# Kernel optimization log

Hardware: AMD Instinct MI355X
Metric: run time of the kernel (lower is better)

## Reference

```python
import jax, jax.numpy as jnp
import numpy as np

E = 8388608          # total edges across batch
G = 2048             # num_graphs
LARGE_NEG = -1.0e9
SCORE_EPS = 1e-6     # self.score_eps
STOP_BIAS = 0.0      # self.stop_logit_bias
RAND_PROB = 0.1      # self.random_action_prob (training)
TEMP = 1.0           # policy_temperature (>= MIN_TEMPERATURE)
PROB_EPS = 1e-12
EPS = float(np.finfo(np.float32).eps)  # torch.finfo(edge_tokens.dtype).eps


def setup_inputs() -> dict:
    key = jax.random.key(0)
    k1, k2, k3, k4, k5 = jax.random.split(key, 5)
    edge_scores = jax.random.uniform(k1, (E,), dtype=jnp.float32)
    edge_residual = jax.random.normal(k2, (E,), dtype=jnp.float32)
    stop_residual = jax.random.normal(k3, (G,), dtype=jnp.float32)
    valid_edges = jax.random.bernoulli(k4, 0.9, (E,))
    edge_batch = jnp.sort(jax.random.randint(k5, (E,), 0, G, dtype=jnp.int32))
    return {"edge_scores": edge_scores, "edge_residual": edge_residual,
            "stop_residual": stop_residual, "valid_edges": valid_edges,
            "edge_batch": edge_batch}


def _segment_log_probs(edge_logits, stop_logits, valid, edge_batch, temp):
    """Faithful port of _log_probs_from_logits: per-graph stable softmax over
    a ragged set of edge logits plus one stop logit per graph."""
    masked = jnp.where(valid, edge_logits, LARGE_NEG)
    scaled = masked / temp                                   # [E]
    sstop = stop_logits / temp                               # [G]
    max_edge = jax.ops.segment_max(scaled, edge_batch, num_segments=G)
    has_edge = jax.ops.segment_sum(jnp.ones_like(scaled), edge_batch, num_segments=G) > 0
    max_edge = jnp.where(has_edge, max_edge, LARGE_NEG)
    max_joint = jnp.maximum(max_edge, sstop)                 # [G]
    exp_edges = jax.ops.segment_sum(jnp.exp(scaled - max_joint[edge_batch]),
                                    edge_batch, num_segments=G)
    exp_stop = jnp.exp(sstop - max_joint)
    log_denom = max_joint + jnp.log(exp_edges + exp_stop + EPS)  # [G]
    log_edge = jnp.where(valid, scaled - log_denom[edge_batch], LARGE_NEG)
    log_stop = sstop - log_denom
    return log_edge, log_stop


def reference(edge_scores, edge_residual, stop_residual, valid_edges, edge_batch):
    # base (prior) distribution from GNN edge scores + stop bias
    base_edge_logits = jnp.log(jnp.maximum(edge_scores, SCORE_EPS))
    base_stop_logits = jnp.full((G,), STOP_BIAS, dtype=jnp.float32)
    base_log_edge, base_log_stop = _segment_log_probs(
        base_edge_logits, base_stop_logits, valid_edges, edge_batch, 1.0)
    # combine with policy residuals and renormalize at temperature
    combined_edge = base_log_edge + edge_residual
    combined_stop = base_log_stop + stop_residual
    clean_log_edge, clean_log_stop = _segment_log_probs(
        combined_edge, combined_stop, valid_edges, edge_batch, TEMP)
    clean_edge_prob = jnp.exp(clean_log_edge)
    clean_stop_prob = jnp.exp(clean_log_stop)
    # uniform random-action mixing
    valid_counts = jax.ops.segment_sum(valid_edges.astype(jnp.float32),
                                       edge_batch, num_segments=G)
    total_actions = jnp.maximum(valid_counts + 1.0, 1.0)     # [G]
    uniform_edge = jnp.where(valid_edges, 1.0 / total_actions[edge_batch], 0.0)
    uniform_stop = 1.0 / total_actions
    sample_edge = (1.0 - RAND_PROB) * clean_edge_prob + RAND_PROB * uniform_edge
    sample_stop = (1.0 - RAND_PROB) * clean_stop_prob + RAND_PROB * uniform_stop
    log_sample_edge = jnp.where(valid_edges,
                                jnp.log(jnp.maximum(sample_edge, PROB_EPS)),
                                LARGE_NEG)
    log_sample_stop = jnp.log(jnp.maximum(sample_stop, PROB_EPS))
    # greedy action per graph: best edge vs stop
    best_val = jax.ops.segment_max(log_sample_edge, edge_batch, num_segments=G)
    idx = jnp.arange(E, dtype=jnp.int32)
    cand = jnp.where(log_sample_edge == best_val[edge_batch], idx, E)
    best_idx = jax.ops.segment_min(cand, edge_batch, num_segments=G)   # [G]
    counts = jax.ops.segment_sum(jnp.ones((E,), jnp.int32), edge_batch, num_segments=G)
    stop_indices = jnp.cumsum(counts)                         # edge_ptr[1:]
    take_stop = log_sample_stop >= best_val
    actions = jnp.where(take_stop, stop_indices, best_idx)
    chosen_edge_lp = clean_log_edge[jnp.minimum(best_idx, E - 1)]
    log_pf = jnp.where(take_stop, clean_log_stop, chosen_edge_lp)     # [G]
    return clean_log_edge, clean_log_stop, actions, log_pf
```

## Files before the change

### kernel.cpp

```cpp
#include <hip/hip_runtime.h>
#include <math.h>
#include <climits>

#define BLOCK 256
#define NCHUNK 5
#define REGCAP (NCHUNK * BLOCK * 4)
#define LARGE_NEG (-1.0e9f)
#define SCORE_EPS 1e-6f
#define RANDP 0.1f
#define PROB_EPS 1e-12f
#define F32EPS 1.1920928955078125e-7f

typedef float f4v __attribute__((ext_vector_type(4)));

__global__ void gfn_setup(const int* __restrict__ batch, int E, int G,
                          int* __restrict__ ptr,
                          const unsigned int* __restrict__ vwords, int nwords,
                          int nbytes, int* __restrict__ flag, int nbPtr) {
  if ((int)blockIdx.x < nbPtr) {
    int g = blockIdx.x * BLOCK + threadIdx.x;
    if (g > G) return;
    int lo = 0, hi = E;
    while (lo < hi) {
      int mid = (lo + hi) >> 1;
      if (batch[mid] < g) lo = mid + 1; else hi = mid;
    }
    ptr[g] = lo;
  } else {
    int c = 0;
    for (int i = threadIdx.x; i < nwords; i += BLOCK) {
      unsigned int w = vwords[i];
      c += ((w & 0x000000FFu) != 0) + ((w & 0x0000FF00u) != 0) +
           ((w & 0x00FF0000u) != 0) + ((w & 0xFF000000u) != 0);
    }
#pragma unroll
    for (int o = 32; o >= 1; o >>= 1) c += __shfl_xor(c, o);
    __shared__ int part[4];
    if ((threadIdx.x & 63) == 0) part[threadIdx.x >> 6] = c;
    __syncthreads();
    if (threadIdx.x == 0) {
      int t = part[0] + part[1] + part[2] + part[3];
      flag[0] = (2 * t > nbytes) ? 1 : 0;
    }
  }
}

__global__ __launch_bounds__(BLOCK) void
gfn_main(const float* __restrict__ scores,
         const float* __restrict__ resid,
         const float* __restrict__ stop_resid,
         const void* __restrict__ validp,
         const int* __restrict__ ptr,
         const int* __restrict__ flag,
         float* __restrict__ out, int E, int G) {
  __shared__ float redf[16];
  __shared__ int redi[4];

  const int g = blockIdx.x;
  const int start = ptr[g];
  const int end = ptr[g + 1];
  const bool byteFmt = (flag[0] != 0);
  const unsigned char* vb = (const unsigned char*)validp;
  const int* vi = (const int*)validp;
  const int abase = start & ~3;

  if ((E & 3) == 0 && (end - abase) <= REGCAP) {
    float c[NCHUNK][4];
    const int t4 = (int)threadIdx.x * 4;

    float smax = 0.f, ssum = 0.f, vc = 0.f, tmax = LARGE_NEG;
#pragma unroll
    for (int j = 0; j < NCHUNK; ++j) {
      const int e0 = abase + j * (BLOCK * 4) + t4;
      if (e0 < end) {
        const float4 s4 = *(const float4*)(scores + e0);
        const float4 r4 = *(const float4*)(resid + e0);
        int vv[4];
        if (byteFmt) {
          const uchar4 u = *(const uchar4*)(vb + e0);
          vv[0] = u.x; vv[1] = u.y; vv[2] = u.z; vv[3] = u.w;
        } else {
          const int4 u = *(const int4*)(vi + e0);
          vv[0] = u.x; vv[1] = u.y; vv[2] = u.z; vv[3] = u.w;
        }
        const float ss[4] = {s4.x, s4.y, s4.z, s4.w};
        const float rr[4] = {r4.x, r4.y, r4.z, r4.w};
#pragma unroll
        for (int k = 0; k < 4; ++k) {
          const int e = e0 + k;
          const bool ok = (e >= start) & (e < end) & (vv[k] != 0);
          const float w = ok ? fmaxf(ss[k], SCORE_EPS) : 0.f;
          smax = fmaxf(smax, w);
          ssum += w;
          vc += ok ? 1.f : 0.f;
          const float t = ok ? (__logf(w) + rr[k]) : LARGE_NEG;
          c[j][k] = t;
          tmax = fmaxf(tmax, t);
        }
      } else {
#pragma unroll
        for (int k = 0; k < 4; ++k) c[j][k] = LARGE_NEG;
      }
    }
#pragma unroll
    for (int o = 32; o >= 1; o >>= 1) {
      smax = fmaxf(smax, __shfl_xor(smax, o));
      ssum += __shfl_xor(ssum, o);
      vc += __shfl_xor(vc, o);
      tmax = fmaxf(tmax, __shfl_xor(tmax, o));
    }
    if ((threadIdx.x & 63) == 0) {
      const int w = threadIdx.x >> 6;
      redf[w] = smax; redf[4 + w] = ssum; redf[8 + w] = vc; redf[12 + w] = tmax;
    }
    __syncthreads();
    smax = fmaxf(fmaxf(redf[0], redf[1]), fmaxf(redf[2], redf[3]));
    ssum = (redf[4] + redf[5]) + (redf[6] + redf[7]);
    vc = (redf[8] + redf[9]) + (redf[10] + redf[11]);
    tmax = fmaxf(fmaxf(redf[12], redf[13]), fmaxf(redf[14], redf[15]));
    __syncthreads();

    const float M = fmaxf(smax, 1.f);
    const float invM = 1.f / M;
    const float ld1 = __logf(M) + __logf(ssum * invM + invM + F32EPS);
    const float m2 = tmax - ld1;
    const float ss2 = stop_resid[g] - ld1;
    const float mj2 = fmaxf(m2, ss2);
    const float off2 = ld1 + mj2;

    float s2 = 0.f;
#pragma unroll
    for (int j = 0; j < NCHUNK; ++j)
#pragma unroll
      for (int k = 0; k < 4; ++k) s2 += __expf(c[j][k] - off2);
#pragma unroll
    for (int o = 32; o >= 1; o >>= 1) s2 += __shfl_xor(s2, o);
    if ((threadIdx.x & 63) == 0) redf[threadIdx.x >> 6] = s2;
    __syncthreads();
    s2 = (redf[0] + redf[1]) + (redf[2] + redf[3]);
    __syncthreads();
    const float ld2 = mj2 + __logf(s2 + __expf(ss2 - mj2) + F32EPS);
    const float clean_stop = ss2 - ld2;
    const float invt = 1.f / fmaxf(vc + 1.f, 1.f);
    const float off3 = ld1 + ld2;

    float bv = -INFINITY;
    int bi = INT_MAX;
#pragma unroll
    for (int j = 0; j < NCHUNK; ++j) {
      const int e0 = abase + j * (BLOCK * 4) + t4;
      if (e0 < end) {
        float ov[4];
#pragma unroll
        for (int k = 0; k < 4; ++k) {
          const int e = e0 + k;
          const float t = c[j][k];
          const bool v = (t != LARGE_NEG);
          ov[k] = v ? (t - off3) : LARGE_NEG;
          if (v && (t > bv || (t == bv && e < bi))) { bv = t; bi = e; }
        }
        if (e0 >= start && e0 + 4 <= end) {
          f4v val; val.x = ov[0]; val.y = ov[1]; val.z = ov[2]; val.w = ov[3];
          __builtin_nontemporal_store(val, (f4v*)(out + e0));
        } else {
#pragma unroll
          for (int k = 0; k < 4; ++k) {
            const int e = e0 + k;
            if (e >= start && e < end)
              __builtin_nontemporal_store(ov[k], out + e);
          }
        }
      }
    }
#pragma unroll
    for (int o = 32; o >= 1; o >>= 1) {
      const float v2 = __shfl_xor(bv, o);
      const int i2 = __shfl_xor(bi, o);
      if (v2 > bv || (v2 == bv && i2 < bi)) { bv = v2; bi = i2; }
    }
    if ((threadIdx.x & 63) == 0) {
      const int w = threadIdx.x >> 6;
      redf[w] = bv; redi[w] = bi;
    }
    __syncthreads();
    if (threadIdx.x == 0) {
      bv = redf[0]; bi = redi[0];
      for (int w = 1; w < 4; ++w) {
        if (redf[w] > bv || (redf[w] == bv && redi[w] < bi)) {
          bv = redf[w]; bi = redi[w];
        }
      }
      const bool anyvalid = (bi != INT_MAX);
      const float wclean = bv - off3;
      float bvls = LARGE_NEG;
      if (anyvalid) {
        const float p = (1.f - RANDP) * __expf(wclean) + RANDP * invt;
        bvls = __logf(fmaxf(p, PROB_EPS));
      }
      const float ssp = (1.f - RANDP) * __expf(clean_stop) + RANDP * invt;
      const float lss = __logf(fmaxf(ssp, PROB_EPS));
      const bool take_stop = (lss >= bvls);
      out[E + g]         = clean_stop;
      out[E + G + g]     = take_stop ? (float)end : (float)bi;
      out[E + 2 * G + g] = take_stop ? clean_stop : wclean;
    }
    return;
  }

  const int n = end - start;
  auto load_l = [&](int e) -> float {
    float s = scores[e];
    int v = byteFmt ? (int)vb[e] : vi[e];
    return v ? __logf(fmaxf(s, SCORE_EPS)) : LARGE_NEG;
  };

  float m1 = LARGE_NEG, vc = 0.f;
  for (int i = threadIdx.x; i < n; i += BLOCK) {
    float l = load_l(start + i);
    m1 = fmaxf(m1, l);
    if (l != LARGE_NEG) vc += 1.f;
  }
#pragma unroll
  for (int o = 32; o >= 1; o >>= 1) {
    m1 = fmaxf(m1, __shfl_xor(m1, o));
    vc += __shfl_xor(vc, o);
  }
  if ((threadIdx.x & 63) == 0) {
    const int w = threadIdx.x >> 6;
    redf[w] = m1; redf[4 + w] = vc;
  }
  __syncthreads();
  m1 = fmaxf(fmaxf(redf[0], redf[1]), fmaxf(redf[2], redf[3]));
  vc = (redf[4] + redf[5]) + (redf[6] + redf[7]);
  __syncthreads();

  const float mj1 = fmaxf(m1, 0.f);
  float s1 = 0.f;
  for (int i = threadIdx.x; i < n; i += BLOCK)
    s1 += __expf(load_l(start + i) - mj1);
#pragma unroll
  for (int o = 32; o >= 1; o >>= 1) s1 += __shfl_xor(s1, o);
  if ((threadIdx.x & 63) == 0) redf[threadIdx.x >> 6] = s1;
  __syncthreads();
  s1 = (redf[0] + redf[1]) + (redf[2] + redf[3]);
  __syncthreads();
  const float ld1 = mj1 + __logf(s1 + __expf(-mj1) + F32EPS);

  float m2 = LARGE_NEG;
  for (int i = threadIdx.x; i < n; i += BLOCK) {
    float l = load_l(start + i);
    float cc = (l != LARGE_NEG) ? (l - ld1 + resid[start + i]) : LARGE_NEG;
    m2 = fmaxf(m2, cc);
  }
#pragma unroll
  for (int o = 32; o >= 1; o >>= 1) m2 = fmaxf(m2, __shfl_xor(m2, o));
  if ((threadIdx.x & 63) == 0) redf[threadIdx.x >> 6] = m2;
  __syncthreads();
  m2 = fmaxf(fmaxf(redf[0], redf[1]), fmaxf(redf[2], redf[3]));
  __syncthreads();

  const float ss2 = stop_resid[g] - ld1;
  const float mj2 = fmaxf(m2, ss2);
  float s2 = 0.f;
  for (int i = threadIdx.x; i < n; i += BLOCK) {
    float l = load_l(start + i);
    float cc = (l != LARGE_NEG) ? (l - ld1 + resid[start + i]) : LARGE_NEG;
    s2 += __expf(cc - mj2);
  }
#pragma unroll
  for (int o = 32; o >= 1; o >>= 1) s2 += __shfl_xor(s2, o);
  if ((threadIdx.x & 63) == 0) redf[threadIdx.x >> 6] = s2;
  __syncthreads();
  s2 = (redf[0] + redf[1]) + (redf[2] + redf[3]);
  __syncthreads();
  const float ld2 = mj2 + __logf(s2 + __expf(ss2 - mj2) + F32EPS);
  const float clean_stop = ss2 - ld2;
  const float invt = 1.f / fmaxf(vc + 1.f, 1.f);

  float bv = -INFINITY; int bi = INT_MAX; float bc = 0.f;
  for (int i = threadIdx.x; i < n; i += BLOCK) {
    const int e = start + i;
    float l = load_l(e);
    float cc = (l != LARGE_NEG) ? (l - ld1 + resid[e]) : LARGE_NEG;
    const bool v = (cc != LARGE_NEG);
    const float clean = cc - ld2;
    out[e] = v ? clean : LARGE_NEG;
    float ls;
    if (v) {
      const float p = (1.f - RANDP) * __expf(clean) + RANDP * invt;
      ls = __logf(fmaxf(p, PROB_EPS));
    } else ls = LARGE_NEG;
    if (ls > bv || (ls == bv && e < bi)) { bv = ls; bi = e; bc = clean; }
  }
#pragma unroll
  for (int o = 32; o >= 1; o >>= 1) {
    const float v2 = __shfl_xor(bv, o);
    const int i2 = __shfl_xor(bi, o);
    const float c2 = __shfl_xor(bc, o);
    if (v2 > bv || (v2 == bv && i2 < bi)) { bv = v2; bi = i2; bc = c2; }
  }
  if ((threadIdx.x & 63) == 0) {
    const int w = threadIdx.x >> 6;
    redf[w] = bv; redf[4 + w] = bc; redi[w] = bi;
  }
  __syncthreads();
  if (threadIdx.x == 0) {
    bv = redf[0]; bi = redi[0]; bc = redf[4];
    for (int w = 1; w < 4; ++w) {
      if (redf[w] > bv || (redf[w] == bv && redi[w] < bi)) {
        bv = redf[w]; bi = redi[w]; bc = redf[4 + w];
      }
    }
    const float ssp = (1.f - RANDP) * __expf(clean_stop) + RANDP * invt;
    const float lss = __logf(fmaxf(ssp, PROB_EPS));
    const bool take_stop = (lss >= bv);
    out[E + g]         = clean_stop;
    out[E + G + g]     = take_stop ? (float)end : (float)bi;
    out[E + 2 * G + g] = take_stop ? clean_stop : bc;
  }
}

extern "C" void kernel_launch(void* const* d_in, const int* in_sizes, int n_in,
                              void* d_out, int out_size, void* d_ws, size_t ws_size,
                              hipStream_t stream) {
  const float* scores     = (const float*)d_in[0];
  const float* resid      = (const float*)d_in[1];
  const float* stop_resid = (const float*)d_in[2];
  const void*  validp     = d_in[3];
  const int*   batch      = (const int*)d_in[4];
  const int E = in_sizes[0];
  const int G = in_sizes[2];

  int* flag = (int*)d_ws;
  int* ptr  = (int*)d_ws + 64;
  float* out = (float*)d_out;

  int sample_bytes = (E < 8192) ? (E & ~3) : 8192;
  int nbPtr = (G + 1 + BLOCK - 1) / BLOCK;
  gfn_setup<<<nbPtr + 1, BLOCK, 0, stream>>>(batch, E, G, ptr,
                                             (const unsigned int*)validp,
                                             sample_bytes / 4, sample_bytes,
                                             flag, nbPtr);
  gfn_main<<<G, BLOCK, 0, stream>>>(scores, resid, stop_resid, validp, ptr,
                                    flag, out, E, G);
}
```

Baseline: 37.15 us.

## Fuse segment-boundary search and format detection into main kernel

Removes the separate setup kernel. Each block now finds its own segment boundaries with a 64-way wave-cooperative search over the sorted batch array, and detects the validity format from a smaller sample inside the block. Loads are hoisted ahead of compute with a compact validity bitmask, launch bounds request higher occupancy, and nontemporal stores become plain stores. This saves one kernel launch and a dependency, but every block repeats the boundary search and format sampling, and the changed occupancy hint may raise register pressure.

```diff
diff --git a/kernel.cpp b/kernel.cpp
--- a/kernel.cpp
+++ b/kernel.cpp
@@ -11,95 +11,116 @@
 #define PROB_EPS 1e-12f
 #define F32EPS 1.1920928955078125e-7f
 
-typedef float f4v __attribute__((ext_vector_type(4)));
-
-__global__ void gfn_setup(const int* __restrict__ batch, int E, int G,
-                          int* __restrict__ ptr,
-                          const unsigned int* __restrict__ vwords, int nwords,
-                          int nbytes, int* __restrict__ flag, int nbPtr) {
-  if ((int)blockIdx.x < nbPtr) {
-    int g = blockIdx.x * BLOCK + threadIdx.x;
-    if (g > G) return;
-    int lo = 0, hi = E;
-    while (lo < hi) {
-      int mid = (lo + hi) >> 1;
-      if (batch[mid] < g) lo = mid + 1; else hi = mid;
-    }
-    ptr[g] = lo;
-  } else {
-    int c = 0;
-    for (int i = threadIdx.x; i < nwords; i += BLOCK) {
-      unsigned int w = vwords[i];
-      c += ((w & 0x000000FFu) != 0) + ((w & 0x0000FF00u) != 0) +
-           ((w & 0x00FF0000u) != 0) + ((w & 0xFF000000u) != 0);
-    }
-#pragma unroll
-    for (int o = 32; o >= 1; o >>= 1) c += __shfl_xor(c, o);
-    __shared__ int part[4];
-    if ((threadIdx.x & 63) == 0) part[threadIdx.x >> 6] = c;
-    __syncthreads();
-    if (threadIdx.x == 0) {
-      int t = part[0] + part[1] + part[2] + part[3];
-      flag[0] = (2 * t > nbytes) ? 1 : 0;
-    }
-  }
+__device__ __forceinline__ int wave_lower_bound(const int* __restrict__ batch,
+                                                int E, int target) {
+  const int lane = (int)(threadIdx.x & 63);
+  long long lo = 0, hi = E;
+  for (int it = 0; it < 12 && hi > lo; ++it) {
+    const long long W = hi - lo;
+    const long long step = (W + 63) >> 6;
+    const long long p = lo + (long long)lane * step;
+    bool pred = false;
+    if (p < hi) pred = (batch[p] < target);
+    const unsigned long long m = __ballot(pred);
+    const int c = __popcll(m);
+    if (c == 0) { hi = lo; break; }
+    const long long plast = lo + (long long)(c - 1) * step;
+    const long long pnext = lo + (long long)c * step;
+    lo = plast + 1;
+    hi = (c < 64 && pnext < hi) ? pnext : hi;
+  }
+  return (int)lo;
 }
 
-__global__ __launch_bounds__(BLOCK) void
+__global__ __launch_bounds__(BLOCK, 4) void
 gfn_main(const float* __restrict__ scores,
          const float* __restrict__ resid,
          const float* __restrict__ stop_resid,
          const void* __restrict__ validp,
-         const int* __restrict__ ptr,
-         const int* __restrict__ flag,
+         const int* __restrict__ batch,
          float* __restrict__ out, int E, int G) {
   __shared__ float redf[16];
   __shared__ int redi[4];
+  __shared__ int sb[2];
+  __shared__ int sflag;
 
   const int g = blockIdx.x;
-  const int start = ptr[g];
-  const int end = ptr[g + 1];
-  const bool byteFmt = (flag[0] != 0);
   const unsigned char* vb = (const unsigned char*)validp;
   const int* vi = (const int*)validp;
+
+  const int wid = (int)(threadIdx.x >> 6);
+  const int lane = (int)(threadIdx.x & 63);
+  if (wid == 0) {
+    const int r = wave_lower_bound(batch, E, g);
+    if (lane == 0) sb[0] = r;
+  } else if (wid == 1) {
+    const int r = wave_lower_bound(batch, E, g + 1);
+    if (lane == 0) sb[1] = r;
+  } else if (wid == 2) {
+    const unsigned int* vwords = (const unsigned int*)validp;
+    const int sampleBytes = (E < 1024) ? (E & ~3) : 1024;
+    const int nwords = sampleBytes >> 2;
+    int cnt = 0;
+    for (int w = lane; w < nwords; w += 64) {
+      const unsigned int x = vwords[w];
+      cnt += ((x & 0x000000FFu) != 0) + ((x & 0x0000FF00u) != 0) +
+             ((x & 0x00FF0000u) != 0) + ((x & 0xFF000000u) != 0);
+    }
+#pragma unroll
+    for (int o = 32; o >= 1; o >>= 1) cnt += __shfl_xor(cnt, o);
+    if (lane == 0) sflag = (2 * cnt > sampleBytes) ? 1 : 0;
+  }
+  __syncthreads();
+  const int start = sb[0];
+  const int end = sb[1];
+  const bool byteFmt = (sflag != 0);
   const int abase = start & ~3;
 
   if ((E & 3) == 0 && (end - abase) <= REGCAP) {
-    float c[NCHUNK][4];
     const int t4 = (int)threadIdx.x * 4;
 
-    float smax = 0.f, ssum = 0.f, vc = 0.f, tmax = LARGE_NEG;
+    float4 s4[NCHUNK], r4[NCHUNK];
+    unsigned int vm[NCHUNK];
 #pragma unroll
     for (int j = 0; j < NCHUNK; ++j) {
       const int e0 = abase + j * (BLOCK * 4) + t4;
+      vm[j] = 0u;
       if (e0 < end) {
-        const float4 s4 = *(const float4*)(scores + e0);
-        const float4 r4 = *(const float4*)(resid + e0);
-        int vv[4];
+        s4[j] = *(const float4*)(scores + e0);
+        r4[j] = *(const float4*)(resid + e0);
         if (byteFmt) {
-          const uchar4 u = *(const uchar4*)(vb + e0);
-          vv[0] = u.x; vv[1] = u.y; vv[2] = u.z; vv[3] = u.w;
+          const unsigned int u = *(const unsigned int*)(vb + e0);
+          vm[j] = ((u & 0x000000FFu) ? 1u : 0u) | ((u & 0x0000FF00u) ? 2u : 0u) |
+                  ((u & 0x00FF0000u) ? 4u : 0u) | ((u & 0xFF000000u) ? 8u : 0u);
         } else {
           const int4 u = *(const int4*)(vi + e0);
-          vv[0] = u.x; vv[1] = u.y; vv[2] = u.z; vv[3] = u.w;
-        }
-        const float ss[4] = {s4.x, s4.y, s4.z, s4.w};
-        const float rr[4] = {r4.x, r4.y, r4.z, r4.w};
-#pragma unroll
-        for (int k = 0; k < 4; ++k) {
-          const int e = e0 + k;
-          const bool ok = (e >= start) & (e < end) & (vv[k] != 0);
-          const float w = ok ? fmaxf(ss[k], SCORE_EPS) : 0.f;
-          smax = fmaxf(smax, w);
-          ssum += w;
-          vc += ok ? 1.f : 0.f;
-          const float t = ok ? (__logf(w) + rr[k]) : LARGE_NEG;
-          c[j][k] = t;
-          tmax = fmaxf(tmax, t);
+          vm[j] = (u.x ? 1u : 0u) | (u.y ? 2u : 0u) |
+                  (u.z ? 4u : 0u) | (u.w ? 8u : 0u);
         }
       } else {
-#pragma unroll
-        for (int k = 0; k < 4; ++k) c[j][k] = LARGE_NEG;
+        s4[j] = make_float4(0.f, 0.f, 0.f, 0.f);
+        r4[j] = make_float4(0.f, 0.f, 0.f, 0.f);
+      }
+    }
+
+    float c[NCHUNK][4];
+    float smax = 0.f, ssum = 0.f, vc = 0.f, tmax = LARGE_NEG;
+#pragma unroll
+    for (int j = 0; j < NCHUNK; ++j) {
+      const int e0 = abase + j * (BLOCK * 4) + t4;
+      const float ss[4] = {s4[j].x, s4[j].y, s4[j].z, s4[j].w};
+      const float rr[4] = {r4[j].x, r4[j].y, r4[j].z, r4[j].w};
+#pragma unroll
+      for (int k = 0; k < 4; ++k) {
+        const int e = e0 + k;
+        const bool ok = ((vm[j] >> k) & 1u) && (e >= start) && (e < end);
+        const float w = ok ? fmaxf(ss[k], SCORE_EPS) : 0.f;
+        smax = fmaxf(smax, w);
+        ssum += w;
+        vc += ok ? 1.f : 0.f;
+        const float t = ok ? (__logf(w) + rr[k]) : LARGE_NEG;
+        c[j][k] = t;
+        tmax = fmaxf(tmax, t);
       }
     }
 #pragma unroll
@@ -109,9 +130,9 @@
       vc += __shfl_xor(vc, o);
       tmax = fmaxf(tmax, __shfl_xor(tmax, o));
     }
-    if ((threadIdx.x & 63) == 0) {
-      const int w = threadIdx.x >> 6;
-      redf[w] = smax; redf[4 + w] = ssum; redf[8 + w] = vc; redf[12 + w] = tmax;
+    if (lane == 0) {
+      redf[wid] = smax; redf[4 + wid] = ssum; redf[8 + wid] = vc;
+      redf[12 + wid] = tmax;
     }
     __syncthreads();
     smax = fmaxf(fmaxf(redf[0], redf[1]), fmaxf(redf[2], redf[3]));
@@ -135,7 +156,7 @@
       for (int k = 0; k < 4; ++k) s2 += __expf(c[j][k] - off2);
 #pragma unroll
     for (int o = 32; o >= 1; o >>= 1) s2 += __shfl_xor(s2, o);
-    if ((threadIdx.x & 63) == 0) redf[threadIdx.x >> 6] = s2;
+    if (lane == 0) redf[wid] = s2;
     __syncthreads();
     s2 = (redf[0] + redf[1]) + (redf[2] + redf[3]);
     __syncthreads();
@@ -160,14 +181,12 @@
           if (v && (t > bv || (t == bv && e < bi))) { bv = t; bi = e; }
         }
         if (e0 >= start && e0 + 4 <= end) {
-          f4v val; val.x = ov[0]; val.y = ov[1]; val.z = ov[2]; val.w = ov[3];
-          __builtin_nontemporal_store(val, (f4v*)(out + e0));
+          *(float4*)(out + e0) = make_float4(ov[0], ov[1], ov[2], ov[3]);
         } else {
 #pragma unroll
           for (int k = 0; k < 4; ++k) {
             const int e = e0 + k;
-            if (e >= start && e < end)
-              __builtin_nontemporal_store(ov[k], out + e);
+            if (e >= start && e < end) out[e] = ov[k];
           }
         }
       }
@@ -178,10 +197,7 @@
       const int i2 = __shfl_xor(bi, o);
       if (v2 > bv || (v2 == bv && i2 < bi)) { bv = v2; bi = i2; }
     }
-    if ((threadIdx.x & 63) == 0) {
-      const int w = threadIdx.x >> 6;
-      redf[w] = bv; redi[w] = bi;
-    }
+    if (lane == 0) { redf[wid] = bv; redi[wid] = bi; }
     __syncthreads();
     if (threadIdx.x == 0) {
       bv = redf[0]; bi = redi[0];
@@ -225,10 +241,7 @@
     m1 = fmaxf(m1, __shfl_xor(m1, o));
     vc += __shfl_xor(vc, o);
   }
-  if ((threadIdx.x & 63) == 0) {
-    const int w = threadIdx.x >> 6;
-    redf[w] = m1; redf[4 + w] = vc;
-  }
+  if (lane == 0) { redf[wid] = m1; redf[4 + wid] = vc; }
   __syncthreads();
   m1 = fmaxf(fmaxf(redf[0], redf[1]), fmaxf(redf[2], redf[3]));
   vc = (redf[4] + redf[5]) + (redf[6] + redf[7]);
@@ -240,7 +253,7 @@
     s1 += __expf(load_l(start + i) - mj1);
 #pragma unroll
   for (int o = 32; o >= 1; o >>= 1) s1 += __shfl_xor(s1, o);
-  if ((threadIdx.x & 63) == 0) redf[threadIdx.x >> 6] = s1;
+  if (lane == 0) redf[wid] = s1;
   __syncthreads();
   s1 = (redf[0] + redf[1]) + (redf[2] + redf[3]);
   __syncthreads();
@@ -254,7 +267,7 @@
   }
 #pragma unroll
   for (int o = 32; o >= 1; o >>= 1) m2 = fmaxf(m2, __shfl_xor(m2, o));
-  if ((threadIdx.x & 63) == 0) redf[threadIdx.x >> 6] = m2;
+  if (lane == 0) redf[wid] = m2;
   __syncthreads();
   m2 = fmaxf(fmaxf(redf[0], redf[1]), fmaxf(redf[2], redf[3]));
   __syncthreads();
@@ -269,7 +282,7 @@
   }
 #pragma unroll
   for (int o = 32; o >= 1; o >>= 1) s2 += __shfl_xor(s2, o);
-  if ((threadIdx.x & 63) == 0) redf[threadIdx.x >> 6] = s2;
+  if (lane == 0) redf[wid] = s2;
   __syncthreads();
   s2 = (redf[0] + redf[1]) + (redf[2] + redf[3]);
   __syncthreads();
@@ -299,10 +312,7 @@
     const float c2 = __shfl_xor(bc, o);
     if (v2 > bv || (v2 == bv && i2 < bi)) { bv = v2; bi = i2; bc = c2; }
   }
-  if ((threadIdx.x & 63) == 0) {
-    const int w = threadIdx.x >> 6;
-    redf[w] = bv; redf[4 + w] = bc; redi[w] = bi;
-  }
+  if (lane == 0) { redf[wid] = bv; redf[4 + wid] = bc; redi[wid] = bi; }
   __syncthreads();
   if (threadIdx.x == 0) {
     bv = redf[0]; bi = redi[0]; bc = redf[4];
@@ -331,16 +341,6 @@
   const int E = in_sizes[0];
   const int G = in_sizes[2];
 
-  int* flag = (int*)d_ws;
-  int* ptr  = (int*)d_ws + 64;
-  float* out = (float*)d_out;
-
-  int sample_bytes = (E < 8192) ? (E & ~3) : 8192;
-  int nbPtr = (G + 1 + BLOCK - 1) / BLOCK;
-  gfn_setup<<<nbPtr + 1, BLOCK, 0, stream>>>(batch, E, G, ptr,
-                                             (const unsigned int*)validp,
-                                             sample_bytes / 4, sample_bytes,
-                                             flag, nbPtr);
-  gfn_main<<<G, BLOCK, 0, stream>>>(scores, resid, stop_resid, validp, ptr,
-                                    flag, out, E, G);
+  gfn_main<<<G, BLOCK, 0, stream>>>(scores, resid, stop_resid, validp, batch,
+                                    (float*)d_out, E, G);
 }
```

New measurement: 39.62 us. +6.7%, slower.

## Stage scores and residuals into LDS via async global_load_lds before compute

Applied to the files above, without the earlier changes.

The fast path now stages each graph's score and residual slices into shared memory with direct global-to-LDS loads, while validity bits are packed into per-chunk bitmasks in registers. It then computes from LDS after a waitcnt and a barrier. Output stores switch from nontemporal to plain stores, and launch bounds request four blocks per CU. The aim is to issue all global loads up front for more memory-level parallelism. In exchange it uses about 40KB of LDS per block, which may limit occupancy, and adds extra barriers.

```diff
diff --git a/kernel.cpp b/kernel.cpp
--- a/kernel.cpp
+++ b/kernel.cpp
@@ -4,14 +4,18 @@
 
 #define BLOCK 256
 #define NCHUNK 5
-#define REGCAP (NCHUNK * BLOCK * 4)
+#define LDSN (NCHUNK * BLOCK * 4)
 #define LARGE_NEG (-1.0e9f)
 #define SCORE_EPS 1e-6f
 #define RANDP 0.1f
 #define PROB_EPS 1e-12f
 #define F32EPS 1.1920928955078125e-7f
 
-typedef float f4v __attribute__((ext_vector_type(4)));
+__device__ __forceinline__ void stage16(const void* g, void* l) {
+  __builtin_amdgcn_global_load_lds(
+      (const __attribute__((address_space(1))) void*)g,
+      (__attribute__((address_space(3))) void*)l, 16, 0, 0);
+}
 
 __global__ void gfn_setup(const int* __restrict__ batch, int E, int G,
                           int* __restrict__ ptr,
@@ -45,7 +49,7 @@
   }
 }
 
-__global__ __launch_bounds__(BLOCK) void
+__global__ __launch_bounds__(BLOCK, 4) void
 gfn_main(const float* __restrict__ scores,
          const float* __restrict__ resid,
          const float* __restrict__ stop_resid,
@@ -53,8 +57,10 @@
          const int* __restrict__ ptr,
          const int* __restrict__ flag,
          float* __restrict__ out, int E, int G) {
-  __shared__ float redf[16];
-  __shared__ int redi[4];
+  __shared__ float sS[LDSN];
+  __shared__ float sR[LDSN];
+  float* const redf = sS;
+  int* const redi = (int*)(sS + 16);
 
   const int g = blockIdx.x;
   const int start = ptr[g];
@@ -63,32 +69,56 @@
   const unsigned char* vb = (const unsigned char*)validp;
   const int* vi = (const int*)validp;
   const int abase = start & ~3;
-
-  if ((E & 3) == 0 && (end - abase) <= REGCAP) {
-    float c[NCHUNK][4];
+  const int wid = (int)(threadIdx.x >> 6);
+  const int lane = (int)(threadIdx.x & 63);
+
+  if ((E & 3) == 0 && (end - abase) <= LDSN) {
     const int t4 = (int)threadIdx.x * 4;
 
-    float smax = 0.f, ssum = 0.f, vc = 0.f, tmax = LARGE_NEG;
+    for (int ci = wid; ci < 4 * NCHUNK; ci += 4) {
+      const int base = ci * 256;
+      const int gidx = abase + base + lane * 4;
+      if (gidx < end) {
+        stage16(scores + gidx, &sS[base]);
+        stage16(resid + gidx, &sR[base]);
+      }
+    }
+
+    unsigned int vm[NCHUNK];
 #pragma unroll
     for (int j = 0; j < NCHUNK; ++j) {
-      const int e0 = abase + j * (BLOCK * 4) + t4;
+      const int e0 = abase + j * 1024 + t4;
+      vm[j] = 0u;
       if (e0 < end) {
-        const float4 s4 = *(const float4*)(scores + e0);
-        const float4 r4 = *(const float4*)(resid + e0);
-        int vv[4];
         if (byteFmt) {
-          const uchar4 u = *(const uchar4*)(vb + e0);
-          vv[0] = u.x; vv[1] = u.y; vv[2] = u.z; vv[3] = u.w;
+          const unsigned int u = *(const unsigned int*)(vb + e0);
+          vm[j] = ((u & 0x000000FFu) ? 1u : 0u) | ((u & 0x0000FF00u) ? 2u : 0u) |
+                  ((u & 0x00FF0000u) ? 4u : 0u) | ((u & 0xFF000000u) ? 8u : 0u);
         } else {
           const int4 u = *(const int4*)(vi + e0);
-          vv[0] = u.x; vv[1] = u.y; vv[2] = u.z; vv[3] = u.w;
-        }
+          vm[j] = (u.x ? 1u : 0u) | (u.y ? 2u : 0u) |
+                  (u.z ? 4u : 0u) | (u.w ? 8u : 0u);
+        }
+      }
+    }
+
+    asm volatile("s_waitcnt vmcnt(0)" ::: "memory");
+    __syncthreads();
+
+    float c[NCHUNK][4];
+    float smax = 0.f, ssum = 0.f, vc = 0.f, tmax = LARGE_NEG;
+#pragma unroll
+    for (int j = 0; j < NCHUNK; ++j) {
+      const int e0 = abase + j * 1024 + t4;
+      if (e0 < end) {
+        const float4 s4 = *(const float4*)&sS[j * 1024 + t4];
+        const float4 r4 = *(const float4*)&sR[j * 1024 + t4];
         const float ss[4] = {s4.x, s4.y, s4.z, s4.w};
         const float rr[4] = {r4.x, r4.y, r4.z, r4.w};
 #pragma unroll
         for (int k = 0; k < 4; ++k) {
           const int e = e0 + k;
-          const bool ok = (e >= start) & (e < end) & (vv[k] != 0);
+          const bool ok = ((vm[j] >> k) & 1u) && (e >= start) && (e < end);
           const float w = ok ? fmaxf(ss[k], SCORE_EPS) : 0.f;
           smax = fmaxf(smax, w);
           ssum += w;
@@ -102,6 +132,7 @@
         for (int k = 0; k < 4; ++k) c[j][k] = LARGE_NEG;
       }
     }
+    __syncthreads();
 #pragma unroll
     for (int o = 32; o >= 1; o >>= 1) {
       smax = fmaxf(smax, __shfl_xor(smax, o));
@@ -109,9 +140,9 @@
       vc += __shfl_xor(vc, o);
       tmax = fmaxf(tmax, __shfl_xor(tmax, o));
     }
-    if ((threadIdx.x & 63) == 0) {
-      const int w = threadIdx.x >> 6;
-      redf[w] = smax; redf[4 + w] = ssum; redf[8 + w] = vc; redf[12 + w] = tmax;
+    if (lane == 0) {
+      redf[wid] = smax; redf[4 + wid] = ssum; redf[8 + wid] = vc;
+      redf[12 + wid] = tmax;
     }
     __syncthreads();
     smax = fmaxf(fmaxf(redf[0], redf[1]), fmaxf(redf[2], redf[3]));
@@ -135,7 +166,7 @@
       for (int k = 0; k < 4; ++k) s2 += __expf(c[j][k] - off2);
 #pragma unroll
     for (int o = 32; o >= 1; o >>= 1) s2 += __shfl_xor(s2, o);
-    if ((threadIdx.x & 63) == 0) redf[threadIdx.x >> 6] = s2;
+    if (lane == 0) redf[wid] = s2;
     __syncthreads();
     s2 = (redf[0] + redf[1]) + (redf[2] + redf[3]);
     __syncthreads();
@@ -148,7 +179,7 @@
     int bi = INT_MAX;
 #pragma unroll
     for (int j = 0; j < NCHUNK; ++j) {
-      const int e0 = abase + j * (BLOCK * 4) + t4;
+      const int e0 = abase + j * 1024 + t4;
       if (e0 < end) {
         float ov[4];
 #pragma unroll
@@ -160,14 +191,12 @@
           if (v && (t > bv || (t == bv && e < bi))) { bv = t; bi = e; }
         }
         if (e0 >= start && e0 + 4 <= end) {
-          f4v val; val.x = ov[0]; val.y = ov[1]; val.z = ov[2]; val.w = ov[3];
-          __builtin_nontemporal_store(val, (f4v*)(out + e0));
+          *(float4*)(out + e0) = make_float4(ov[0], ov[1], ov[2], ov[3]);
         } else {
 #pragma unroll
           for (int k = 0; k < 4; ++k) {
             const int e = e0 + k;
-            if (e >= start && e < end)
-              __builtin_nontemporal_store(ov[k], out + e);
+            if (e >= start && e < end) out[e] = ov[k];
           }
         }
       }
@@ -178,10 +207,7 @@
       const int i2 = __shfl_xor(bi, o);
       if (v2 > bv || (v2 == bv && i2 < bi)) { bv = v2; bi = i2; }
     }
-    if ((threadIdx.x & 63) == 0) {
-      const int w = threadIdx.x >> 6;
-      redf[w] = bv; redi[w] = bi;
-    }
+    if (lane == 0) { redf[wid] = bv; redi[wid] = bi; }
     __syncthreads();
     if (threadIdx.x == 0) {
       bv = redf[0]; bi = redi[0];
@@ -225,10 +251,7 @@
     m1 = fmaxf(m1, __shfl_xor(m1, o));
     vc += __shfl_xor(vc, o);
   }
-  if ((threadIdx.x & 63) == 0) {
-    const int w = threadIdx.x >> 6;
-    redf[w] = m1; redf[4 + w] = vc;
-  }
+  if (lane == 0) { redf[wid] = m1; redf[4 + wid] = vc; }
   __syncthreads();
   m1 = fmaxf(fmaxf(redf[0], redf[1]), fmaxf(redf[2], redf[3]));
   vc = (redf[4] + redf[5]) + (redf[6] + redf[7]);
@@ -240,7 +263,7 @@
     s1 += __expf(load_l(start + i) - mj1);
 #pragma unroll
   for (int o = 32; o >= 1; o >>= 1) s1 += __shfl_xor(s1, o);
-  if ((threadIdx.x & 63) == 0) redf[threadIdx.x >> 6] = s1;
+  if (lane == 0) redf[wid] = s1;
   __syncthreads();
   s1 = (redf[0] + redf[1]) + (redf[2] + redf[3]);
   __syncthreads();
@@ -254,7 +277,7 @@
   }
 #pragma unroll
   for (int o = 32; o >= 1; o >>= 1) m2 = fmaxf(m2, __shfl_xor(m2, o));
-  if ((threadIdx.x & 63) == 0) redf[threadIdx.x >> 6] = m2;
+  if (lane == 0) redf[wid] = m2;
   __syncthreads();
   m2 = fmaxf(fmaxf(redf[0], redf[1]), fmaxf(redf[2], redf[3]));
   __syncthreads();
@@ -269,7 +292,7 @@
   }
 #pragma unroll
   for (int o = 32; o >= 1; o >>= 1) s2 += __shfl_xor(s2, o);
-  if ((threadIdx.x & 63) == 0) redf[threadIdx.x >> 6] = s2;
+  if (lane == 0) redf[wid] = s2;
   __syncthreads();
   s2 = (redf[0] + redf[1]) + (redf[2] + redf[3]);
   __syncthreads();
@@ -299,10 +322,7 @@
     const float c2 = __shfl_xor(bc, o);
     if (v2 > bv || (v2 == bv && i2 < bi)) { bv = v2; bi = i2; bc = c2; }
   }
-  if ((threadIdx.x & 63) == 0) {
-    const int w = threadIdx.x >> 6;
-    redf[w] = bv; redf[4 + w] = bc; redi[w] = bi;
-  }
+  if (lane == 0) { redf[wid] = bv; redf[4 + wid] = bc; redi[wid] = bi; }
   __syncthreads();
   if (threadIdx.x == 0) {
     bv = redf[0]; bi = redi[0]; bc = redf[4];
```

Measured after the change: 46.61 us. +25.5%, slower.
